# Kernel tuning notes

Measured on AMD Instinct MI355X. Metric: run time of the kernel, lower is better.

The kernel has to match this reference:

```python
import jax, jax.numpy as jnp
import numpy as np

KS = 32        # kernel_size (chunk size)
STRIDE = 16    # kernel_stride
H = 8          # head_num_k
D = 128        # head_dim
B = 4          # number of sequences
SEQ = 8192     # tokens per sequence (equal-length varlen batch)


def setup_inputs() -> dict:
    key = jax.random.key(0)
    k1, k2, k3, k4, k5 = jax.random.split(key, 5)
    kv = jax.random.normal(k1, (B * SEQ, 2, H, D), dtype=jnp.float32)
    cu_seqlens = jnp.arange(B + 1, dtype=jnp.int32) * SEQ
    # torch Conv1d default init: uniform(-s, s), s = 1/sqrt(in_channels*kernel_size)
    s = 1.0 / np.sqrt(D * KS)
    k_conv_w = jax.random.uniform(k2, (D, D, KS), jnp.float32, -s, s)
    k_conv_b = jax.random.uniform(k3, (D,), jnp.float32, -s, s)
    v_conv_w = jax.random.uniform(k4, (D, D, KS), jnp.float32, -s, s)
    v_conv_b = jax.random.uniform(k5, (D,), jnp.float32, -s, s)
    return {"kv": kv, "cu_seqlens": cu_seqlens,
            "k_conv_w": k_conv_w, "k_conv_b": k_conv_b,
            "v_conv_w": v_conv_w, "v_conv_b": v_conv_b}


def _chunk_indices(cu_seqlens, total_tokens):
    # Equal-length sequences: every strided chunk is valid, so shapes are static.
    batch = cu_seqlens.shape[0] - 1
    seqlen = total_tokens // batch
    nc = (seqlen - KS) // STRIDE + 1  # chunks per sequence
    starts = cu_seqlens[:-1].astype(jnp.int32)          # [B]
    offs = (jnp.arange(nc, dtype=jnp.int32) * STRIDE)   # [nc]
    pos = jnp.arange(KS, dtype=jnp.int32)               # [KS]
    idx = starts[:, None, None] + offs[None, :, None] + pos[None, None, :]  # [B, nc, KS]
    cu_comp = jnp.arange(batch + 1, dtype=jnp.int32) * nc
    return idx.reshape(batch * nc, KS), cu_comp


def reference(kv, cu_seqlens, k_conv_w, k_conv_b, v_conv_w, v_conv_b):
    idx, cu_comp = _chunk_indices(cu_seqlens, kv.shape[0])  # [L, KS]
    filtered = kv[idx.reshape(-1)].reshape(idx.shape[0], KS, 2, H, D)  # [L, KS, 2, H, D]
    k = filtered[:, :, 0]  # [L, KS, H, D]
    v = filtered[:, :, 1]
    # Conv1d with kernel spanning the whole chunk -> single output position:
    # out[l,h,o] = sum_{i,t} x[l,t,h,i] * W[o,i,t] + b[o]
    compress_k = jnp.einsum('lthi,oit->lho', k, k_conv_w) + k_conv_b
    compress_v = jnp.einsum('lthi,oit->lho', v, v_conv_w) + v_conv_b
    return compress_k, compress_v, cu_comp
```

## Files before the change

kernel.cpp:

```cpp
#include <hip/hip_runtime.h>

typedef __attribute__((ext_vector_type(8))) short bf16x8;
typedef __attribute__((ext_vector_type(4))) float f32x4;

#define MFMA16(A, B, C) __builtin_amdgcn_mfma_f32_16x16x32_bf16(A, B, C, 0, 0, 0)

__device__ __forceinline__ unsigned short f2bf(float f) {
  union { float f; unsigned int u; } v; v.f = f;
  return (unsigned short)((v.u + 0x7fffu + ((v.u >> 16) & 1u)) >> 16);
}
#define PK(LO, HI) (((unsigned int)f2bf(LO)) | ((unsigned int)f2bf(HI) << 16))

__global__ void cu_kernel(const int* __restrict__ cu_in, float* __restrict__ out,
                          int cubase, int nb, int strideh) {
  int t = threadIdx.x;
  if (t <= nb) out[cubase + t] = (float)(cu_in[t] / strideh);
}

__global__ __launch_bounds__(256) void prep_kernel(
    const float* __restrict__ kw, const float* __restrict__ vw,
    unsigned short* __restrict__ imgK, unsigned short* __restrict__ imgV, int KSd) {
  __shared__ float wlds[4096];
  int tid = threadIdx.x, bid = blockIdx.x;
  int sel = bid >> 7, o = bid & 127;
  int nel = 128 * KSd;
  const float* wo = (sel ? vw : kw) + (size_t)o * nel;
  unsigned short* dst = sel ? imgV : imgK;
  for (int i = tid; i < (nel >> 2); i += 256)
    ((float4*)wlds)[i] = ((const float4*)wo)[i];
  __syncthreads();
  int swE = (o & 7) << 3;
  for (int idx = tid; idx < nel; idx += 256) {
    int s = idx >> 6, c = idx & 63;
    int i = ((s & 1) << 6) + (c ^ swE);
    dst[((size_t)s << 13) + (o << 6) + c] = f2bf(wlds[i * KSd + (s >> 1)]);
  }
}

__global__ __launch_bounds__(512) void gemm_hybrid_kernel(
    const float* __restrict__ kv,
    const float* __restrict__ biasK, const float* __restrict__ biasV,
    const unsigned short* __restrict__ imgK, const unsigned short* __restrict__ imgV,
    float* __restrict__ out,
    int vbase, int nc, int ltot, int tokmax, int seqb, int mtiles) {
  __shared__ __align__(16) unsigned short T[2][66 * 128];
  __shared__ __align__(16) unsigned short Bs[2][8192];
  int tid = threadIdx.x, bid = blockIdx.x;
  int per_sel = 8 * mtiles;
  int sel = (bid >= per_sel) ? 1 : 0;
  int rem = bid - sel * per_sel;
  int h = rem / mtiles, mtile = rem - h * mtiles;
  int m0 = mtile * 64;
  const unsigned short* img = sel ? imgV : imgK;
  const float* bias = sel ? biasV : biasK;
  int outbase = sel ? vbase : 0;
  int lane = tid & 63, wid = tid >> 6;
  int warpM = wid >> 2, warpN = wid & 3;
  int l15 = lane & 15, l4 = lane >> 4;

  int b0 = m0 / nc, c0 = m0 - b0 * nc;
  int btok0 = b0 * seqb + c0 * 16;
  int rb = (b0 + 1) * nc - m0; if (rb > 64) rb = 64;

  int sjl = tid >> 4, sje = tid & 15;
  int soff = sel * 1024 + h * 128 + sje * 8;
  int js0 = sjl, js1 = 32 + sjl, js2 = 64 + sjl;

  int kb0 = l4 * 16;
  int r0 = warpM * 32 + l15, r1 = r0 + 16;
  int j0 = r0 + (r0 >= rb ? 1 : 0);
  int j1 = r1 + (r1 >= rb ? 1 : 0);
  int jb00 = j0 * 256,       jsw00 = (j0 & 7) << 4;
  int jb01 = (j0 + 1) * 256, jsw01 = ((j0 + 1) & 7) << 4;
  int jb10 = j1 * 256,       jsw10 = (j1 & 7) << 4;
  int jb11 = (j1 + 1) * 256, jsw11 = ((j1 + 1) & 7) << 4;

  int o0 = warpN * 32 + l15, o1 = o0 + 16;
  int brb0 = o0 * 128, bsw0 = (o0 & 7) << 4;
  int brb1 = o1 * 128, bsw1 = (o1 & 7) << 4;

  f32x4 zz = {0.f, 0.f, 0.f, 0.f};
  f32x4 acc00 = zz, acc01 = zz, acc10 = zz, acc11 = zz;
  float4 ta0, ta1, ta2, tb0, tb1, tb2;
  uint4 Br0, Br1;

#define STAGE_LOAD(P) do {                                                       \
    int t0_ = btok0 + js0 * 16 + (P); if (t0_ > tokmax) t0_ = tokmax;            \
    const float* a0_ = kv + ((size_t)t0_ << 11) + soff;                          \
    ta0 = *(const float4*)a0_; tb0 = *(const float4*)(a0_ + 4);                  \
    int t1_ = btok0 + js1 * 16 + (P); if (t1_ > tokmax) t1_ = tokmax;            \
    const float* a1_ = kv + ((size_t)t1_ << 11) + soff;                          \
    ta1 = *(const float4*)a1_; tb1 = *(const float4*)(a1_ + 4);                  \
    if (sjl < 2) {                                                               \
      int t2_ = btok0 + js2 * 16 + (P); if (t2_ > tokmax) t2_ = tokmax;          \
      const float* a2_ = kv + ((size_t)t2_ << 11) + soff;                        \
      ta2 = *(const float4*)a2_; tb2 = *(const float4*)(a2_ + 4);                \
    }                                                                            \
  } while (0)

#define T_WRITE(TB) do {                                                         \
    char* tp_ = (char*)(TB);                                                     \
    *(uint4*)(tp_ + js0 * 256 + ((sje * 16) ^ ((js0 & 7) << 4))) =               \
      make_uint4(PK(ta0.x, ta0.y), PK(ta0.z, ta0.w), PK(tb0.x, tb0.y), PK(tb0.z, tb0.w)); \
    *(uint4*)(tp_ + js1 * 256 + ((sje * 16) ^ ((js1 & 7) << 4))) =               \
      make_uint4(PK(ta1.x, ta1.y), PK(ta1.z, ta1.w), PK(tb1.x, tb1.y), PK(tb1.z, tb1.w)); \
    if (sjl < 2)                                                                 \
      *(uint4*)(tp_ + js2 * 256 + ((sje * 16) ^ ((js2 & 7) << 4))) =             \
        make_uint4(PK(ta2.x, ta2.y), PK(ta2.z, ta2.w), PK(tb2.x, tb2.y), PK(tb2.z, tb2.w)); \
  } while (0)

#define B_LOAD(S) do {                                                           \
    const uint4* bsrc_ = (const uint4*)(img + ((size_t)(S) << 13));              \
    Br0 = bsrc_[tid];                                                            \
    Br1 = bsrc_[512 + tid];                                                      \
  } while (0)

#define B_WRITE(DB) do {                                                         \
    uint4* bdst_ = (uint4*)Bs[DB];                                               \
    bdst_[tid] = Br0;                                                            \
    bdst_[512 + tid] = Br1;                                                      \
  } while (0)

#define SUBSTEP(HF, JB0, JSW0, JB1, JSW1, BB) do {                               \
    const char* tc_ = (const char*)T[tcur];                                      \
    const char* bc_ = (const char*)Bs[BB];                                       \
    _Pragma("unroll")                                                            \
    for (int kk = 0; kk < 2; ++kk) {                                             \
      int kcA_ = (HF) * 128 + kk * 64 + kb0;                                     \
      int kcB_ = kk * 64 + kb0;                                                  \
      bf16x8 a0_ = *(const bf16x8*)(tc_ + (JB0) + (kcA_ ^ (JSW0)));              \
      bf16x8 a1_ = *(const bf16x8*)(tc_ + (JB1) + (kcA_ ^ (JSW1)));              \
      bf16x8 b0_ = *(const bf16x8*)(bc_ + brb0 + (kcB_ ^ bsw0));                 \
      bf16x8 b1_ = *(const bf16x8*)(bc_ + brb1 + (kcB_ ^ bsw1));                 \
      acc00 = MFMA16(a0_, b0_, acc00);                                           \
      acc01 = MFMA16(a0_, b1_, acc01);                                           \
      acc10 = MFMA16(a1_, b0_, acc10);                                           \
      acc11 = MFMA16(a1_, b1_, acc11);                                           \
    }                                                                            \
  } while (0)

  int tcur = 0;
  STAGE_LOAD(0);
  T_WRITE(T[0]);
  B_LOAD(0);
  B_WRITE(0);
  __syncthreads();

  int bcur = 0;
  for (int p = 0; p < 16; ++p) {
    B_LOAD(2 * p + 1);
    if (p < 15) STAGE_LOAD(p + 1);
    SUBSTEP(0, jb00, jsw00, jb10, jsw10, bcur);
    B_WRITE(bcur ^ 1);
    __syncthreads(); bcur ^= 1;
    B_LOAD(2 * p + 32);
    SUBSTEP(1, jb00, jsw00, jb10, jsw10, bcur);
    B_WRITE(bcur ^ 1);
    __syncthreads(); bcur ^= 1;
    B_LOAD(2 * p + 33);
    SUBSTEP(0, jb01, jsw01, jb11, jsw11, bcur);
    B_WRITE(bcur ^ 1);
    __syncthreads(); bcur ^= 1;
    if (p < 15) B_LOAD(2 * p + 2);
    SUBSTEP(1, jb01, jsw01, jb11, jsw11, bcur);
    if (p < 15) {
      T_WRITE(T[tcur ^ 1]);
      B_WRITE(bcur ^ 1);
    }
    __syncthreads(); bcur ^= 1; tcur ^= 1;
  }

#define STORE_Q(ACC, MI, NI) do {                                                \
    int o_ = warpN * 32 + (NI) * 16 + l15;                                       \
    float bv_ = bias[o_];                                                        \
    int lb_ = m0 + warpM * 32 + (MI) * 16 + l4 * 4;                              \
    _Pragma("unroll")                                                            \
    for (int jj = 0; jj < 4; ++jj) {                                             \
      int ll_ = lb_ + jj;                                                        \
      if (ll_ < ltot)                                                            \
        out[(size_t)outbase + (size_t)ll_ * 1024 + h * 128 + o_] = ACC[jj] + bv_; \
    }                                                                            \
  } while (0)
  STORE_Q(acc00, 0, 0); STORE_Q(acc01, 0, 1);
  STORE_Q(acc10, 1, 0); STORE_Q(acc11, 1, 1);
}

__global__ __launch_bounds__(512) void gemm_kernel(
    const float* __restrict__ kv,
    const float* __restrict__ biasK, const float* __restrict__ biasV,
    const unsigned short* __restrict__ imgK, const unsigned short* __restrict__ imgV,
    const float* __restrict__ kw, const float* __restrict__ vw,
    float* __restrict__ out,
    int selbase, int vbase, int nc, int ltot, int nsteps,
    int tokmax, int seqb, int strideh, int KSd, int mtiles) {
  __shared__ __align__(16) unsigned short As[2][4096];
  __shared__ __align__(16) unsigned short Bsf[2][8192];
  int tid = threadIdx.x, bid = blockIdx.x;
  int per_sel = 8 * mtiles;
  int sel = selbase + (bid >= per_sel);
  int rem = (bid >= per_sel) ? bid - per_sel : bid;
  int h = rem / mtiles, mtile = rem - h * mtiles;
  int m0 = mtile * 64;
  const unsigned short* img = sel ? imgV : imgK;
  const float* bias = sel ? biasV : biasK;
  const float* wsel = sel ? vw : kw;
  int outbase = sel ? vbase : 0;
  int lane = tid & 63, wid = tid >> 6;
  int warpM = wid >> 2, warpN = wid & 3;

  int aj = tid & 7, r = tid >> 3;
  int l = m0 + r; if (l > ltot - 1) l = ltot - 1;
  int b = l / nc, c = l - b * nc;
  int btok = b * seqb + c * strideh;
  const float* abase = kv + sel * 1024 + h * 128 + aj * 4;
  int swr = (r & 7) << 3;
  int awb0 = r * 128 + 2 * ((aj * 4) ^ swr);
  int awb1 = r * 128 + 2 * ((aj * 4 + 32) ^ swr);

  int o_g = tid >> 3, cb_g = (tid & 7) << 3;
  int ib_g = cb_g ^ ((o_g & 7) << 3);
  const float* g0 = wsel + (size_t)o_g * (KSd << 7);
  const float* g1 = g0 + ((size_t)64 * (KSd << 7));

  int kb0 = (lane >> 4) * 16;
  int arb[2], asw[2], brb[2], bsw[2];
#pragma unroll
  for (int mi = 0; mi < 2; ++mi) {
    int rr = warpM * 32 + mi * 16 + (lane & 15);
    arb[mi] = rr * 128; asw[mi] = (rr & 7) << 4;
  }
#pragma unroll
  for (int ni = 0; ni < 2; ++ni) {
    int oo = warpN * 32 + ni * 16 + (lane & 15);
    brb[ni] = oo * 128; bsw[ni] = (oo & 7) << 4;
  }

  f32x4 acc[2][2];
  f32x4 zz = {0.f, 0.f, 0.f, 0.f};
#pragma unroll
  for (int a = 0; a < 2; ++a)
#pragma unroll
    for (int b2 = 0; b2 < 2; ++b2) acc[a][b2] = zz;

  float4 Af0, Af1;
  uint4 Brr[2];

#define LOAD_STEP(S) do {                                                        \
    int tok_ = btok + ((S) >> 1); if (tok_ > tokmax) tok_ = tokmax;              \
    const float* ap_ = abase + ((size_t)tok_ << 11) + (((S) & 1) << 6);          \
    Af0 = *(const float4*)ap_;                                                   \
    Af1 = *(const float4*)(ap_ + 32);                                            \
    if (img) {                                                                   \
      const uint4* bsrc_ = (const uint4*)(img + ((size_t)(S) << 13));            \
      Brr[0] = bsrc_[tid];                                                       \
      Brr[1] = bsrc_[512 + tid];                                                 \
    } else {                                                                     \
      int t_ = (S) >> 1, i0_ = (((S) & 1) << 6) + ib_g;                          \
      unsigned int p0_[4], p1_[4];                                               \
      _Pragma("unroll")                                                          \
      for (int m = 0; m < 4; ++m) {                                              \
        p0_[m] = (unsigned int)f2bf(g0[(i0_ + 2*m) * KSd + t_])                  \
               | ((unsigned int)f2bf(g0[(i0_ + 2*m + 1) * KSd + t_]) << 16);     \
        p1_[m] = (unsigned int)f2bf(g1[(i0_ + 2*m) * KSd + t_])                  \
               | ((unsigned int)f2bf(g1[(i0_ + 2*m + 1) * KSd + t_]) << 16);     \
      }                                                                          \
      Brr[0] = make_uint4(p0_[0], p0_[1], p0_[2], p0_[3]);                       \
      Brr[1] = make_uint4(p1_[0], p1_[1], p1_[2], p1_[3]);                       \
    }                                                                            \
  } while (0)

#define WRITE_STEP(DB) do {                                                      \
    *(uint2*)((char*)As[DB] + awb0) = make_uint2(PK(Af0.x, Af0.y), PK(Af0.z, Af0.w)); \
    *(uint2*)((char*)As[DB] + awb1) = make_uint2(PK(Af1.x, Af1.y), PK(Af1.z, Af1.w)); \
    uint4* bdst_ = (uint4*)Bsf[DB];                                              \
    bdst_[tid] = Brr[0];                                                         \
    bdst_[512 + tid] = Brr[1];                                                   \
  } while (0)

#define COMPUTE_STEP(CB) do {                                                    \
    _Pragma("unroll")                                                            \
    for (int kk = 0; kk < 2; ++kk) {                                             \
      bf16x8 af_[2], bg_[2];                                                     \
      int kc_ = kk * 64 + kb0;                                                   \
      _Pragma("unroll")                                                          \
      for (int mi = 0; mi < 2; ++mi)                                             \
        af_[mi] = *(const bf16x8*)((const char*)As[CB] + arb[mi] + (kc_ ^ asw[mi])); \
      _Pragma("unroll")                                                          \
      for (int ni = 0; ni < 2; ++ni)                                             \
        bg_[ni] = *(const bf16x8*)((const char*)Bsf[CB] + brb[ni] + (kc_ ^ bsw[ni])); \
      _Pragma("unroll")                                                          \
      for (int mi = 0; mi < 2; ++mi)                                             \
      _Pragma("unroll")                                                          \
        for (int ni = 0; ni < 2; ++ni)                                           \
          acc[mi][ni] = MFMA16(af_[mi], bg_[ni], acc[mi][ni]);                   \
    }                                                                            \
  } while (0)

  LOAD_STEP(0);
  WRITE_STEP(0);
  __syncthreads();
  int cur = 0;
  for (int s = 0; s < nsteps; ++s) {
    if (s + 1 < nsteps) LOAD_STEP(s + 1);
    COMPUTE_STEP(cur);
    if (s + 1 < nsteps) WRITE_STEP(cur ^ 1);
    __syncthreads();
    cur ^= 1;
  }

  int l15 = lane & 15, l4 = lane >> 4;
#pragma unroll
  for (int ni = 0; ni < 2; ++ni) {
    int o = warpN * 32 + ni * 16 + l15;
    float bv = bias[o];
#pragma unroll
    for (int mi = 0; mi < 2; ++mi) {
      int lb = m0 + warpM * 32 + mi * 16 + l4 * 4;
      f32x4 v = acc[mi][ni];
#pragma unroll
      for (int jj = 0; jj < 4; ++jj) {
        int ll = lb + jj;
        if (ll < ltot)
          out[(size_t)outbase + (size_t)ll * 1024 + h * 128 + o] = v[jj] + bv;
      }
    }
  }
}

extern "C" void kernel_launch(void* const* d_in, const int* in_sizes, int n_in,
                              void* d_out, int out_size, void* d_ws, size_t ws_size,
                              hipStream_t stream) {
  long kvN = 0; int kvi = 0;
  for (int i = 0; i < n_in; ++i)
    if ((long)in_sizes[i] > kvN) { kvN = in_sizes[i]; kvi = i; }
  const float* kv = (const float*)d_in[kvi];
  const float *w0 = nullptr, *w1 = nullptr, *b0 = nullptr, *b1 = nullptr;
  const int* cuin = nullptr;
  int KSd = 32, nb = 4;
  for (int i = 0; i < n_in; ++i) {
    if (i == kvi) continue;
    int sz = in_sizes[i];
    if (sz == 128) { if (!b0) b0 = (const float*)d_in[i]; else if (!b1) b1 = (const float*)d_in[i]; }
    else if (sz <= 32) { nb = sz - 1; cuin = (const int*)d_in[i]; }
    else if (sz >= 4096) {
      if (!w0) { w0 = (const float*)d_in[i]; KSd = sz / 16384; }
      else if (!w1) w1 = (const float*)d_in[i];
    }
  }
  if (!w0) w0 = (const float*)d_in[2];
  if (!b0) b0 = (const float*)d_in[3];
  if (!w1) w1 = (const float*)d_in[4];
  if (!b1) b1 = (const float*)d_in[5];
  if (!cuin) cuin = (const int*)d_in[1];
  if (nb < 1) nb = 4;

  float* out = (float*)d_out;

  int cubase  = out_size - (nb + 1);
  int vbase   = cubase >> 1;
  int ltot    = cubase >> 11;
  int nc      = ltot / nb;
  int nsteps  = 2 * KSd;
  long tokens = kvN >> 11;
  int seqb    = (int)(tokens / nb);
  int strideh = (nc > 1) ? (seqb - KSd) / (nc - 1) : KSd;
  int tokmax  = (int)tokens - 1;
  int mtiles  = (ltot + 63) >> 6;
  int per_sel = 8 * mtiles;

  cu_kernel<<<1, 64, 0, stream>>>(cuin, out, cubase, nb, strideh);

  size_t imgel = (size_t)nsteps * 8192;
  size_t imgbytes = imgel * 2;
  bool fast = (KSd == 32) && (strideh == 16) && (nc >= 64) &&
              (ws_size >= 2 * imgbytes);
  if (fast) {
    unsigned short* imgK = (unsigned short*)d_ws;
    unsigned short* imgV = imgK + imgel;
    prep_kernel<<<256, 256, 0, stream>>>(w0, w1, imgK, imgV, KSd);
    gemm_hybrid_kernel<<<2 * per_sel, 512, 0, stream>>>(
        kv, b0, b1, imgK, imgV, out, vbase, nc, ltot, tokmax, seqb, mtiles);
  } else if (ws_size >= 2 * imgbytes) {
    unsigned short* imgK = (unsigned short*)d_ws;
    unsigned short* imgV = imgK + imgel;
    prep_kernel<<<256, 256, 0, stream>>>(w0, w1, imgK, imgV, KSd);
    gemm_kernel<<<2 * per_sel, 512, 0, stream>>>(kv, b0, b1, imgK, imgV, w0, w1, out,
        0, vbase, nc, ltot, nsteps, tokmax, seqb, strideh, KSd, mtiles);
  } else {
    gemm_kernel<<<2 * per_sel, 512, 0, stream>>>(kv, b0, b1,
        (const unsigned short*)nullptr, (const unsigned short*)nullptr, w0, w1, out,
        0, vbase, nc, ltot, nsteps, tokmax, seqb, strideh, KSd, mtiles);
  }
}
```

Before: 87.54 us.

## Load weight fragments directly into registers and split K across warps

The fast-path GEMM no longer stages the weight image through double-buffered shared memory. Each wave loads its bf16 B fragments straight from global memory into registers, using an unswizzled image layout from prep_kernel. Warps are now split along K instead of M: each wave covers all 64 rows for half the K slice, and the two partial results are summed through shared memory at the end. This cuts the per-substep barriers from four to one per chunk step and frees the B LDS buffers. The cost is more per-wave global/L2 traffic for weights and a final cross-warp reduction.

After: 117.7 us. +34.5%, slower.

```diff
diff --git a/kernel.cpp b/kernel.cpp
--- a/kernel.cpp
+++ b/kernel.cpp
@@ -19,7 +19,8 @@
 
 __global__ __launch_bounds__(256) void prep_kernel(
     const float* __restrict__ kw, const float* __restrict__ vw,
-    unsigned short* __restrict__ imgK, unsigned short* __restrict__ imgV, int KSd) {
+    unsigned short* __restrict__ imgK, unsigned short* __restrict__ imgV,
+    int KSd, int dosw) {
   __shared__ float wlds[4096];
   int tid = threadIdx.x, bid = blockIdx.x;
   int sel = bid >> 7, o = bid & 127;
@@ -29,7 +30,7 @@
   for (int i = tid; i < (nel >> 2); i += 256)
     ((float4*)wlds)[i] = ((const float4*)wo)[i];
   __syncthreads();
-  int swE = (o & 7) << 3;
+  int swE = dosw ? ((o & 7) << 3) : 0;
   for (int idx = tid; idx < nel; idx += 256) {
     int s = idx >> 6, c = idx & 63;
     int i = ((s & 1) << 6) + (c ^ swE);
@@ -37,14 +38,13 @@
   }
 }
 
-__global__ __launch_bounds__(512) void gemm_hybrid_kernel(
+__global__ __launch_bounds__(512) void gemm_breg_kernel(
     const float* __restrict__ kv,
     const float* __restrict__ biasK, const float* __restrict__ biasV,
     const unsigned short* __restrict__ imgK, const unsigned short* __restrict__ imgV,
     float* __restrict__ out,
     int vbase, int nc, int ltot, int tokmax, int seqb, int mtiles) {
   __shared__ __align__(16) unsigned short T[2][66 * 128];
-  __shared__ __align__(16) unsigned short Bs[2][8192];
   int tid = threadIdx.x, bid = blockIdx.x;
   int per_sel = 8 * mtiles;
   int sel = (bid >= per_sel) ? 1 : 0;
@@ -55,7 +55,7 @@
   const float* bias = sel ? biasV : biasK;
   int outbase = sel ? vbase : 0;
   int lane = tid & 63, wid = tid >> 6;
-  int warpM = wid >> 2, warpN = wid & 3;
+  int ngrp = wid & 3, kw = wid >> 2;
   int l15 = lane & 15, l4 = lane >> 4;
 
   int b0 = m0 / nc, c0 = m0 - b0 * nc;
@@ -66,23 +66,27 @@
   int soff = sel * 1024 + h * 128 + sje * 8;
   int js0 = sjl, js1 = 32 + sjl, js2 = 64 + sjl;
 
-  int kb0 = l4 * 16;
-  int r0 = warpM * 32 + l15, r1 = r0 + 16;
-  int j0 = r0 + (r0 >= rb ? 1 : 0);
-  int j1 = r1 + (r1 >= rb ? 1 : 0);
-  int jb00 = j0 * 256,       jsw00 = (j0 & 7) << 4;
-  int jb01 = (j0 + 1) * 256, jsw01 = ((j0 + 1) & 7) << 4;
-  int jb10 = j1 * 256,       jsw10 = (j1 & 7) << 4;
-  int jb11 = (j1 + 1) * 256, jsw11 = ((j1 + 1) & 7) << 4;
-
-  int o0 = warpN * 32 + l15, o1 = o0 + 16;
-  int brb0 = o0 * 128, bsw0 = (o0 & 7) << 4;
-  int brb1 = o1 * 128, bsw1 = (o1 & 7) << 4;
+  int kb = kw * 64 + l4 * 16;
+  int jbL[4], jswL[4], jbH[4], jswH[4];
+#pragma unroll
+  for (int mi = 0; mi < 4; ++mi) {
+    int r = mi * 16 + l15;
+    int j = r + (r >= rb ? 1 : 0);
+    jbL[mi] = j * 256;       jswL[mi] = (j & 7) << 4;
+    jbH[mi] = (j + 1) * 256; jswH[mi] = ((j + 1) & 7) << 4;
+  }
+
+  int o0 = ngrp * 32 + l15;
+  size_t bo0 = (size_t)o0 * 64 + kw * 32 + l4 * 8;
+  size_t bo1 = (size_t)(o0 + 16) * 64 + kw * 32 + l4 * 8;
+#define BFRAG(S, OFF) (*(const bf16x8*)(img + ((size_t)(S) << 13) + (OFF)))
 
   f32x4 zz = {0.f, 0.f, 0.f, 0.f};
-  f32x4 acc00 = zz, acc01 = zz, acc10 = zz, acc11 = zz;
+  f32x4 acc[4][2];
+#pragma unroll
+  for (int mi = 0; mi < 4; ++mi) { acc[mi][0] = zz; acc[mi][1] = zz; }
+
   float4 ta0, ta1, ta2, tb0, tb1, tb2;
-  uint4 Br0, Br1;
 
 #define STAGE_LOAD(P) do {                                                       \
     int t0_ = btok0 + js0 * 16 + (P); if (t0_ > tokmax) t0_ = tokmax;            \
@@ -109,80 +113,75 @@
         make_uint4(PK(ta2.x, ta2.y), PK(ta2.z, ta2.w), PK(tb2.x, tb2.y), PK(tb2.z, tb2.w)); \
   } while (0)
 
-#define B_LOAD(S) do {                                                           \
-    const uint4* bsrc_ = (const uint4*)(img + ((size_t)(S) << 13));              \
-    Br0 = bsrc_[tid];                                                            \
-    Br1 = bsrc_[512 + tid];                                                      \
-  } while (0)
-
-#define B_WRITE(DB) do {                                                         \
-    uint4* bdst_ = (uint4*)Bs[DB];                                               \
-    bdst_[tid] = Br0;                                                            \
-    bdst_[512 + tid] = Br1;                                                      \
-  } while (0)
-
-#define SUBSTEP(HF, JB0, JSW0, JB1, JSW1, BB) do {                               \
-    const char* tc_ = (const char*)T[tcur];                                      \
-    const char* bc_ = (const char*)Bs[BB];                                       \
+#define SUBSTEP(HF, JB, JSW, B0, B1, TC) do {                                    \
+    const char* tc_ = (const char*)(TC);                                         \
+    int kc_ = (HF) * 128 + kb;                                                   \
+    bf16x8 a_[4];                                                                \
     _Pragma("unroll")                                                            \
-    for (int kk = 0; kk < 2; ++kk) {                                             \
-      int kcA_ = (HF) * 128 + kk * 64 + kb0;                                     \
-      int kcB_ = kk * 64 + kb0;                                                  \
-      bf16x8 a0_ = *(const bf16x8*)(tc_ + (JB0) + (kcA_ ^ (JSW0)));              \
-      bf16x8 a1_ = *(const bf16x8*)(tc_ + (JB1) + (kcA_ ^ (JSW1)));              \
-      bf16x8 b0_ = *(const bf16x8*)(bc_ + brb0 + (kcB_ ^ bsw0));                 \
-      bf16x8 b1_ = *(const bf16x8*)(bc_ + brb1 + (kcB_ ^ bsw1));                 \
-      acc00 = MFMA16(a0_, b0_, acc00);                                           \
-      acc01 = MFMA16(a0_, b1_, acc01);                                           \
-      acc10 = MFMA16(a1_, b0_, acc10);                                           \
-      acc11 = MFMA16(a1_, b1_, acc11);                                           \
+    for (int mi = 0; mi < 4; ++mi)                                               \
+      a_[mi] = *(const bf16x8*)(tc_ + JB[mi] + (kc_ ^ JSW[mi]));                 \
+    _Pragma("unroll")                                                            \
+    for (int mi = 0; mi < 4; ++mi) {                                             \
+      acc[mi][0] = MFMA16(a_[mi], B0, acc[mi][0]);                               \
+      acc[mi][1] = MFMA16(a_[mi], B1, acc[mi][1]);                               \
     }                                                                            \
   } while (0)
 
-  int tcur = 0;
   STAGE_LOAD(0);
   T_WRITE(T[0]);
-  B_LOAD(0);
-  B_WRITE(0);
+  bf16x8 cA0 = BFRAG(0, bo0), cA1 = BFRAG(0, bo1);
+  bf16x8 cB0 = BFRAG(1, bo0), cB1 = BFRAG(1, bo1);
   __syncthreads();
 
-  int bcur = 0;
   for (int p = 0; p < 16; ++p) {
-    B_LOAD(2 * p + 1);
+    int s2 = 2 * p;
     if (p < 15) STAGE_LOAD(p + 1);
-    SUBSTEP(0, jb00, jsw00, jb10, jsw10, bcur);
-    B_WRITE(bcur ^ 1);
-    __syncthreads(); bcur ^= 1;
-    B_LOAD(2 * p + 32);
-    SUBSTEP(1, jb00, jsw00, jb10, jsw10, bcur);
-    B_WRITE(bcur ^ 1);
-    __syncthreads(); bcur ^= 1;
-    B_LOAD(2 * p + 33);
-    SUBSTEP(0, jb01, jsw01, jb11, jsw11, bcur);
-    B_WRITE(bcur ^ 1);
-    __syncthreads(); bcur ^= 1;
-    if (p < 15) B_LOAD(2 * p + 2);
-    SUBSTEP(1, jb01, jsw01, jb11, jsw11, bcur);
+    bf16x8 dA0 = BFRAG(s2 + 32, bo0), dA1 = BFRAG(s2 + 32, bo1);
+    bf16x8 dB0 = BFRAG(s2 + 33, bo0), dB1 = BFRAG(s2 + 33, bo1);
+    SUBSTEP(0, jbL, jswL, cA0, cA1, T[p & 1]);
+    bf16x8 nA0, nA1, nB0, nB1;
     if (p < 15) {
-      T_WRITE(T[tcur ^ 1]);
-      B_WRITE(bcur ^ 1);
-    }
-    __syncthreads(); bcur ^= 1; tcur ^= 1;
-  }
-
-#define STORE_Q(ACC, MI, NI) do {                                                \
-    int o_ = warpN * 32 + (NI) * 16 + l15;                                       \
-    float bv_ = bias[o_];                                                        \
-    int lb_ = m0 + warpM * 32 + (MI) * 16 + l4 * 4;                              \
-    _Pragma("unroll")                                                            \
-    for (int jj = 0; jj < 4; ++jj) {                                             \
-      int ll_ = lb_ + jj;                                                        \
-      if (ll_ < ltot)                                                            \
-        out[(size_t)outbase + (size_t)ll_ * 1024 + h * 128 + o_] = ACC[jj] + bv_; \
-    }                                                                            \
-  } while (0)
-  STORE_Q(acc00, 0, 0); STORE_Q(acc01, 0, 1);
-  STORE_Q(acc10, 1, 0); STORE_Q(acc11, 1, 1);
+      nA0 = BFRAG(s2 + 2, bo0); nA1 = BFRAG(s2 + 2, bo1);
+      nB0 = BFRAG(s2 + 3, bo0); nB1 = BFRAG(s2 + 3, bo1);
+    }
+    SUBSTEP(1, jbL, jswL, cB0, cB1, T[p & 1]);
+    SUBSTEP(0, jbH, jswH, dA0, dA1, T[p & 1]);
+    SUBSTEP(1, jbH, jswH, dB0, dB1, T[p & 1]);
+    if (p < 15) {
+      T_WRITE(T[(p + 1) & 1]);
+      cA0 = nA0; cA1 = nA1; cB0 = nB0; cB1 = nB1;
+    }
+    __syncthreads();
+  }
+
+  float* red = (float*)T;
+  if (kw == 1) {
+#pragma unroll
+    for (int mi = 0; mi < 4; ++mi)
+#pragma unroll
+      for (int ni = 0; ni < 2; ++ni)
+        *(f32x4*)(red + ((size_t)((ngrp * 8 + mi * 2 + ni) * 64 + lane)) * 4) = acc[mi][ni];
+  }
+  __syncthreads();
+  if (kw == 0) {
+#pragma unroll
+    for (int ni = 0; ni < 2; ++ni) {
+      int o = ngrp * 32 + ni * 16 + l15;
+      float bv = bias[o];
+#pragma unroll
+      for (int mi = 0; mi < 4; ++mi) {
+        f32x4 other = *(const f32x4*)(red + ((size_t)((ngrp * 8 + mi * 2 + ni) * 64 + lane)) * 4);
+        f32x4 v = acc[mi][ni];
+        int lb = m0 + mi * 16 + l4 * 4;
+#pragma unroll
+        for (int jj = 0; jj < 4; ++jj) {
+          int ll = lb + jj;
+          if (ll < ltot)
+            out[(size_t)outbase + (size_t)ll * 1024 + h * 128 + o] = v[jj] + other[jj] + bv;
+        }
+      }
+    }
+  }
 }
 
 __global__ __launch_bounds__(512) void gemm_kernel(
@@ -377,13 +376,13 @@
   if (fast) {
     unsigned short* imgK = (unsigned short*)d_ws;
     unsigned short* imgV = imgK + imgel;
-    prep_kernel<<<256, 256, 0, stream>>>(w0, w1, imgK, imgV, KSd);
-    gemm_hybrid_kernel<<<2 * per_sel, 512, 0, stream>>>(
+    prep_kernel<<<256, 256, 0, stream>>>(w0, w1, imgK, imgV, KSd, 0);
+    gemm_breg_kernel<<<2 * per_sel, 512, 0, stream>>>(
         kv, b0, b1, imgK, imgV, out, vbase, nc, ltot, tokmax, seqb, mtiles);
   } else if (ws_size >= 2 * imgbytes) {
     unsigned short* imgK = (unsigned short*)d_ws;
     unsigned short* imgV = imgK + imgel;
-    prep_kernel<<<256, 256, 0, stream>>>(w0, w1, imgK, imgV, KSd);
+    prep_kernel<<<256, 256, 0, stream>>>(w0, w1, imgK, imgV, KSd, 1);
     gemm_kernel<<<2 * per_sel, 512, 0, stream>>>(kv, b0, b1, imgK, imgV, w0, w1, out,
         0, vbase, nc, ltot, nsteps, tokmax, seqb, strideh, KSd, mtiles);
   } else {
```

## Deepen weight-tile prefetch to two register sets and fold cu kernel into prep

Applied to the files above, without the earlier changes.

The B-operand weight stream now uses two register sets (A/B), so each global load is issued two substeps ahead of its LDS write instead of one. This hides more global-load latency behind the MFMA substeps. Full __syncthreads is replaced by a custom barrier that waits only on LDS counters, and MFMA sections run at raised wave priority via s_setprio. The separate cu_seqlens launch is merged into prep_kernel to save one kernel launch. The cost is more live registers and a barrier that does not wait for outstanding global loads, so correctness depends on the order of the register uses.

Measured after the change: 77.91 us. 11.0% less time.

```diff
diff --git a/kernel.cpp b/kernel.cpp
--- a/kernel.cpp
+++ b/kernel.cpp
@@ -11,15 +11,18 @@
 }
 #define PK(LO, HI) (((unsigned int)f2bf(LO)) | ((unsigned int)f2bf(HI) << 16))
 
-__global__ void cu_kernel(const int* __restrict__ cu_in, float* __restrict__ out,
-                          int cubase, int nb, int strideh) {
-  int t = threadIdx.x;
-  if (t <= nb) out[cubase + t] = (float)(cu_in[t] / strideh);
-}
+#define BAR() do {                                              \
+    asm volatile("s_waitcnt lgkmcnt(0)" ::: "memory");          \
+    __builtin_amdgcn_s_barrier();                               \
+    asm volatile("" ::: "memory");                              \
+  } while (0)
 
 __global__ __launch_bounds__(256) void prep_kernel(
     const float* __restrict__ kw, const float* __restrict__ vw,
-    unsigned short* __restrict__ imgK, unsigned short* __restrict__ imgV, int KSd) {
+    unsigned short* __restrict__ imgK, unsigned short* __restrict__ imgV,
+    int KSd, int dosw,
+    const int* __restrict__ cuin, float* __restrict__ outf,
+    int cubase, int nb, int strideh) {
   __shared__ float wlds[4096];
   int tid = threadIdx.x, bid = blockIdx.x;
   int sel = bid >> 7, o = bid & 127;
@@ -29,12 +32,13 @@
   for (int i = tid; i < (nel >> 2); i += 256)
     ((float4*)wlds)[i] = ((const float4*)wo)[i];
   __syncthreads();
-  int swE = (o & 7) << 3;
+  int swE = dosw ? ((o & 7) << 3) : 0;
   for (int idx = tid; idx < nel; idx += 256) {
     int s = idx >> 6, c = idx & 63;
     int i = ((s & 1) << 6) + (c ^ swE);
     dst[((size_t)s << 13) + (o << 6) + c] = f2bf(wlds[i * KSd + (s >> 1)]);
   }
+  if (bid == 0 && tid <= nb) outf[cubase + tid] = (float)(cuin[tid] / strideh);
 }
 
 __global__ __launch_bounds__(512) void gemm_hybrid_kernel(
@@ -82,7 +86,7 @@
   f32x4 zz = {0.f, 0.f, 0.f, 0.f};
   f32x4 acc00 = zz, acc01 = zz, acc10 = zz, acc11 = zz;
   float4 ta0, ta1, ta2, tb0, tb1, tb2;
-  uint4 Br0, Br1;
+  uint4 BrA0, BrA1, BrB0, BrB1;
 
 #define STAGE_LOAD(P) do {                                                       \
     int t0_ = btok0 + js0 * 16 + (P); if (t0_ > tokmax) t0_ = tokmax;            \
@@ -109,21 +113,22 @@
         make_uint4(PK(ta2.x, ta2.y), PK(ta2.z, ta2.w), PK(tb2.x, tb2.y), PK(tb2.z, tb2.w)); \
   } while (0)
 
-#define B_LOAD(S) do {                                                           \
+#define B_LOAD(R0, R1, S) do {                                                   \
     const uint4* bsrc_ = (const uint4*)(img + ((size_t)(S) << 13));              \
-    Br0 = bsrc_[tid];                                                            \
-    Br1 = bsrc_[512 + tid];                                                      \
-  } while (0)
-
-#define B_WRITE(DB) do {                                                         \
+    R0 = bsrc_[tid];                                                             \
+    R1 = bsrc_[512 + tid];                                                       \
+  } while (0)
+
+#define B_WRITE(DB, R0, R1) do {                                                 \
     uint4* bdst_ = (uint4*)Bs[DB];                                               \
-    bdst_[tid] = Br0;                                                            \
-    bdst_[512 + tid] = Br1;                                                      \
+    bdst_[tid] = R0;                                                             \
+    bdst_[512 + tid] = R1;                                                       \
   } while (0)
 
 #define SUBSTEP(HF, JB0, JSW0, JB1, JSW1, BB) do {                               \
     const char* tc_ = (const char*)T[tcur];                                      \
     const char* bc_ = (const char*)Bs[BB];                                       \
+    __builtin_amdgcn_s_setprio(1);                                               \
     _Pragma("unroll")                                                            \
     for (int kk = 0; kk < 2; ++kk) {                                             \
       int kcA_ = (HF) * 128 + kk * 64 + kb0;                                     \
@@ -137,37 +142,40 @@
       acc10 = MFMA16(a1_, b0_, acc10);                                           \
       acc11 = MFMA16(a1_, b1_, acc11);                                           \
     }                                                                            \
+    __builtin_amdgcn_s_setprio(0);                                               \
   } while (0)
 
   int tcur = 0;
   STAGE_LOAD(0);
   T_WRITE(T[0]);
-  B_LOAD(0);
-  B_WRITE(0);
-  __syncthreads();
-
-  int bcur = 0;
+  B_LOAD(BrA0, BrA1, 0);
+  B_WRITE(0, BrA0, BrA1);
+  B_LOAD(BrB0, BrB1, 1);
+  B_LOAD(BrA0, BrA1, 32);
+  BAR();
+
   for (int p = 0; p < 16; ++p) {
-    B_LOAD(2 * p + 1);
     if (p < 15) STAGE_LOAD(p + 1);
-    SUBSTEP(0, jb00, jsw00, jb10, jsw10, bcur);
-    B_WRITE(bcur ^ 1);
-    __syncthreads(); bcur ^= 1;
-    B_LOAD(2 * p + 32);
-    SUBSTEP(1, jb00, jsw00, jb10, jsw10, bcur);
-    B_WRITE(bcur ^ 1);
-    __syncthreads(); bcur ^= 1;
-    B_LOAD(2 * p + 33);
-    SUBSTEP(0, jb01, jsw01, jb11, jsw11, bcur);
-    B_WRITE(bcur ^ 1);
-    __syncthreads(); bcur ^= 1;
-    if (p < 15) B_LOAD(2 * p + 2);
-    SUBSTEP(1, jb01, jsw01, jb11, jsw11, bcur);
+    SUBSTEP(0, jb00, jsw00, jb10, jsw10, 0);
+    B_WRITE(1, BrB0, BrB1);
+    B_LOAD(BrB0, BrB1, 2 * p + 33);
+    BAR();
+    SUBSTEP(1, jb00, jsw00, jb10, jsw10, 1);
+    B_WRITE(0, BrA0, BrA1);
+    if (p < 15) B_LOAD(BrA0, BrA1, 2 * p + 2);
+    BAR();
+    SUBSTEP(0, jb01, jsw01, jb11, jsw11, 0);
+    B_WRITE(1, BrB0, BrB1);
+    if (p < 15) B_LOAD(BrB0, BrB1, 2 * p + 3);
+    BAR();
+    SUBSTEP(1, jb01, jsw01, jb11, jsw11, 1);
     if (p < 15) {
+      B_WRITE(0, BrA0, BrA1);
+      B_LOAD(BrA0, BrA1, 2 * p + 34);
       T_WRITE(T[tcur ^ 1]);
-      B_WRITE(bcur ^ 1);
+      BAR();
     }
-    __syncthreads(); bcur ^= 1; tcur ^= 1;
+    tcur ^= 1;
   }
 
 #define STORE_Q(ACC, MI, NI) do {                                                \
@@ -368,8 +376,6 @@
   int mtiles  = (ltot + 63) >> 6;
   int per_sel = 8 * mtiles;
 
-  cu_kernel<<<1, 64, 0, stream>>>(cuin, out, cubase, nb, strideh);
-
   size_t imgel = (size_t)nsteps * 8192;
   size_t imgbytes = imgel * 2;
   bool fast = (KSd == 32) && (strideh == 16) && (nc >= 64) &&
@@ -377,16 +383,21 @@
   if (fast) {
     unsigned short* imgK = (unsigned short*)d_ws;
     unsigned short* imgV = imgK + imgel;
-    prep_kernel<<<256, 256, 0, stream>>>(w0, w1, imgK, imgV, KSd);
+    prep_kernel<<<256, 256, 0, stream>>>(w0, w1, imgK, imgV, KSd, 1,
+                                         cuin, out, cubase, nb, strideh);
     gemm_hybrid_kernel<<<2 * per_sel, 512, 0, stream>>>(
         kv, b0, b1, imgK, imgV, out, vbase, nc, ltot, tokmax, seqb, mtiles);
   } else if (ws_size >= 2 * imgbytes) {
     unsigned short* imgK = (unsigned short*)d_ws;
     unsigned short* imgV = imgK + imgel;
-    prep_kernel<<<256, 256, 0, stream>>>(w0, w1, imgK, imgV, KSd);
+    prep_kernel<<<256, 256, 0, stream>>>(w0, w1, imgK, imgV, KSd, 1,
+                                         cuin, out, cubase, nb, strideh);
     gemm_kernel<<<2 * per_sel, 512, 0, stream>>>(kv, b0, b1, imgK, imgV, w0, w1, out,
         0, vbase, nc, ltot, nsteps, tokmax, seqb, strideh, KSd, mtiles);
   } else {
+    prep_kernel<<<256, 256, 0, stream>>>(w0, w1, (unsigned short*)d_ws,
+                                         (unsigned short*)d_ws, 0, 1,
+                                         cuin, out, cubase, nb, strideh);
     gemm_kernel<<<2 * per_sel, 512, 0, stream>>>(kv, b0, b1,
         (const unsigned short*)nullptr, (const unsigned short*)nullptr, w0, w1, out,
         0, vbase, nc, ltot, nsteps, tokmax, seqb, strideh, KSd, mtiles);
```
